# Optimization experiments

Measured on AMD Instinct MI355X. Metric: run time of the kernel, lower is better.

## Reference

```python
import jax, jax.numpy as jnp
import numpy as np

NA, NW, H = 20000, 100000, 128
DA, DW = 64, 128
E_CR, E_IN, E_CO = 400000, 600000, 300000


def _seg_softmax(logits, seg, n):
    m = jax.ops.segment_max(logits, seg, num_segments=n)
    e = jnp.exp(logits - m[seg])
    s = jax.ops.segment_sum(e, seg, num_segments=n)
    return e / (s[seg] + 1e-16)


def _gat(x_src, x_dst, edge, W, b, a_s, a_d):
    # PyG GATConv, heads=1, concat=False, shared lin for src/dst, add_self_loops=True
    n_src, n_dst = x_src.shape[0], x_dst.shape[0]
    loops = jnp.arange(min(n_src, n_dst), dtype=edge.dtype)
    src = jnp.concatenate([edge[0], loops])
    dst = jnp.concatenate([edge[1], loops])
    hs = x_src @ W            # [n_src, H]
    hd = x_dst @ W            # [n_dst, H]
    logit = jax.nn.leaky_relu((hs @ a_s)[src] + (hd @ a_d)[dst], 0.2)
    alpha = _seg_softmax(logit, dst, n_dst)          # softmax over in-neighborhoods
    out = jax.ops.segment_sum(alpha[:, None] * hs[src], dst, num_segments=n_dst)
    return out + b


def _mlp2(x, w1, b1, w2, b2):
    return jax.nn.relu(x @ w1 + b1) @ w2 + b2


def setup_inputs() -> dict:
    key = jax.random.key(0)
    ks = iter(jax.random.split(key, 40))

    def p(shape, scale=0.1):
        return jax.random.normal(next(ks), shape, jnp.float32) * scale

    def edges(n_src, n_dst, E):
        s = jax.random.randint(next(ks), (E,), 0, n_src, dtype=jnp.int32)
        d = jax.random.randint(next(ks), (E,), 0, n_dst, dtype=jnp.int32)
        d = jnp.where(s == d, (d + 1) % n_dst, d)  # keep input loop-free (PyG strips them)
        return jnp.stack([s, d])

    e_creates = edges(NA, NW, E_CR)
    inp = {
        'artist_feat': jax.random.normal(next(ks), (NA, DA), jnp.float32),
        'work_feat': jax.random.normal(next(ks), (NW, DW), jnp.float32),
        'a_w1': p((DA, H)), 'a_b1': jnp.zeros(H, jnp.float32),
        'a_w2': p((H, H)), 'a_b2': jnp.zeros(H, jnp.float32),
        'w_w1': p((DW, H)), 'w_b1': jnp.zeros(H, jnp.float32),
        'w_w2': p((H, H)), 'w_b2': jnp.zeros(H, jnp.float32),
        'cr_W': p((H, H)), 'cr_b': jnp.zeros(H, jnp.float32), 'cr_as': p((H,)), 'cr_ad': p((H,)),
        'in_W': p((H, H)), 'in_b': jnp.zeros(H, jnp.float32), 'in_as': p((H,)), 'in_ad': p((H,)),
        'co_W': p((H, H)), 'co_b': jnp.zeros(H, jnp.float32), 'co_as': p((H,)), 'co_ad': p((H,)),
        'p_w1': p((2 * H, 256)), 'p_b1': jnp.zeros(256, jnp.float32),
        'p_w2': p((256, 128)), 'p_b2': jnp.zeros(128, jnp.float32),
        'p_w3': p((128, 1)), 'p_b3': jnp.zeros(1, jnp.float32),
        'e_creates': e_creates,
        'e_created_by': jnp.flip(e_creates, axis=0),  # reverse relation [work, artist]
        'e_infl': edges(NW, NW, E_IN),
        'e_collab': edges(NA, NA, E_CO),
    }
    return inp


def reference(artist_feat, work_feat,
              a_w1, a_b1, a_w2, a_b2,
              w_w1, w_b1, w_w2, w_b2,
              cr_W, cr_b, cr_as, cr_ad,
              in_W, in_b, in_as, in_ad,
              co_W, co_b, co_as, co_ad,
              p_w1, p_b1, p_w2, p_b2, p_w3, p_b3,
              e_creates, e_created_by, e_infl, e_collab):
    ax = _mlp2(artist_feat, a_w1, a_b1, a_w2, a_b2)      # [NA, H]
    wx = _mlp2(work_feat, w_w1, w_b1, w_w2, w_b2)        # [NW, H]
    wx = jax.nn.elu(_gat(ax, wx, e_creates, cr_W, cr_b, cr_as, cr_ad))
    wx = jax.nn.elu(_gat(wx, wx, e_infl, in_W, in_b, in_as, in_ad))
    au = _gat(wx, ax, e_created_by, cr_W, cr_b, cr_as, cr_ad)  # no elu (matches source)
    ac = jax.nn.elu(_gat(au, au, e_collab, co_W, co_b, co_as, co_ad))
    comb = jnp.concatenate([au, ac], axis=1)             # [NA, 2H]
    h = jax.nn.relu(comb @ p_w1 + p_b1)                  # dropout is identity in eval
    h = jax.nn.relu(h @ p_w2 + p_b2)
    return (h @ p_w3 + p_b3).squeeze()
```

## Files before the change

### kernel.cpp

```cpp
#include <hip/hip_runtime.h>
#include <hip/hip_bf16.h>
#include <cstddef>

#define NA 20000
#define NW 100000
#define HH 128
#define DA 64
#define E_CR 400000
#define E_IN 600000
#define E_CO 300000

#define ROW1 0
#define ROW2 (NW)
#define ROW3 (2 * NW)
#define ROW4 (2 * NW + NA)
#define NTOT (2 * NW + 2 * NA)
#define CAPW 40
#define CAPA 88
#define GNB ((NA + 127) / 128)
#define NPREPG (7 * 128)

typedef short v8s __attribute__((ext_vector_type(8)));
typedef float v4f __attribute__((ext_vector_type(4)));

constexpr int PSLOT = 2 * 128 * 264;

__device__ inline short f2bf(float x) {
    union { float f; unsigned u; } c; c.f = x;
    unsigned r = c.u + 0x7fff + ((c.u >> 16) & 1);
    return (short)(r >> 16);
}
__device__ inline float bf2f(short s) {
    union { unsigned u; float f; } c; c.u = ((unsigned)(unsigned short)s) << 16;
    return c.f;
}
__device__ inline float bfu2f(unsigned short s) {
    union { unsigned u; float f; } c; c.u = ((unsigned)s) << 16;
    return c.f;
}

__device__ inline void split8(const float* xv, v8s& h, v8s& l) {
#pragma unroll
    for (int p = 0; p < 4; ++p) {
        float2 xf; xf.x = xv[2 * p]; xf.y = xv[2 * p + 1];
        __hip_bfloat162 hb = __float22bfloat162_rn(xf);
        float2 hf = __bfloat1622float2(hb);
        float2 lf; lf.x = xf.x - hf.x; lf.y = xf.y - hf.y;
        __hip_bfloat162 lb = __float22bfloat162_rn(lf);
        union { __hip_bfloat162 b; short2 s; } uh, ul;
        uh.b = hb; ul.b = lb;
        h[2 * p] = uh.s.x; h[2 * p + 1] = uh.s.y;
        l[2 * p] = ul.s.x; l[2 * p + 1] = ul.s.y;
    }
}

struct AppChunk { const int* e; int E; int* pad; int cap; int* deg; };

__device__ inline void do_append(const AppChunk& ap, int bid) {
    int b0 = bid * 1024 + threadIdx.x;
    int s[4], d[4]; bool ok[4];
#pragma unroll
    for (int u = 0; u < 4; ++u) {
        int i = b0 + u * 256;
        ok[u] = i < ap.E;
        s[u] = 0; d[u] = 0;
        if (ok[u]) { s[u] = ap.e[i]; d[u] = ap.e[ap.E + i]; }
    }
    int p[4];
#pragma unroll
    for (int u = 0; u < 4; ++u) if (ok[u]) p[u] = atomicAdd(&ap.deg[d[u]], 1);
#pragma unroll
    for (int u = 0; u < 4; ++u)
        if (ok[u] && p[u] < ap.cap)
            ap.pad[(size_t)d[u] * ap.cap + p[u]] = s[u];
}

struct PrepDesc { const float* src; int ldw; int K; };
struct PrepArgs {
    PrepDesc d[10];
    const float *wvW, *wvA;
    const float *ww2, *aw2, *wb2, *ab2;
    float *uW, *u3, *cons, *bf;
    short* wf;
    const float* gX; const float* gB; float* gY; int gM;
};

__global__ __launch_bounds__(256) void k_prep_append(PrepArgs a, short* __restrict__ out,
                                                     AppChunk ap)
{
    __shared__ short Bs2[2 * 128 * 72];
    int bx = blockIdx.x;

    if (bx == 0) {
        __shared__ float sv[HH];
        int t = threadIdx.x;
        if (t < HH) {
            float s = 0.f;
            for (int j = 0; j < HH; ++j) s += a.wvW[(size_t)t * HH + j] * a.wvA[j];
            sv[t] = s;
        }
        __syncthreads();
        if (t < HH) {
            float s = 0.f;
            for (int j = 0; j < HH; ++j) s += a.ww2[(size_t)t * HH + j] * sv[j];
            a.uW[t] = s;
        } else {
            int k = t - HH;
            float s = 0.f;
            for (int j = 0; j < HH; ++j) s += a.aw2[(size_t)k * HH + j] * sv[j];
            a.u3[k] = s;
        }
        if (t == 0) {
            float s = 0.f;
            for (int j = 0; j < HH; ++j) s += a.wb2[j] * sv[j];
            a.cons[0] = s;
        }
        if (t == 1) {
            float s = 0.f;
            for (int j = 0; j < HH; ++j) s += a.ab2[j] * sv[j];
            a.cons[1] = s;
        }
        return;
    }
    bx -= 1;
    if (bx < 4) {
        int k = bx * 32 + (threadIdx.x >> 3);
        int cb = (threadIdx.x & 7) * 16;
        for (int c = cb; c < cb + 16; ++c) {
            float s = 0.f;
            for (int j = 0; j < HH; ++j) s += a.aw2[(size_t)k * HH + j] * a.wvW[(size_t)j * HH + c];
            short h = f2bf(s);
            short l = f2bf(s - bf2f(h));
            a.wf[c * 136 + k] = h;
            a.wf[128 * 136 + c * 136 + k] = l;
        }
        if (bx == 0 && threadIdx.x < HH) {
            int c = threadIdx.x;
            float s = 0.f;
            for (int j = 0; j < HH; ++j) s += a.ab2[j] * a.wvW[(size_t)j * HH + c];
            a.bf[c] = s;
        }
        return;
    }
    bx -= 4;
    {
        int n1 = (ap.E + 1023) >> 10;
        if (bx < n1) { do_append(ap, bx); return; }
        bx -= n1;
    }
    if (bx < GNB) {
        const int bid = bx;
        const int tid = threadIdx.x;
        const int wave = tid >> 6, lane = tid & 63;
        const int l15 = lane & 15, quad = lane >> 4;
        const int wrow = bid * 128 + wave * 32;
        for (int e = tid; e < 64 * 128; e += 256) {
            int n = e & 127, k = e >> 7;
            float x = a.d[0].src[(size_t)k * 128 + n];
            short h = f2bf(x);
            short l = f2bf(x - bf2f(h));
            Bs2[n * 72 + k] = h;
            Bs2[128 * 72 + n * 72 + k] = l;
        }
        v8s ah[2][2], al[2][2];
#pragma unroll
        for (int rf = 0; rf < 2; ++rf) {
            int r = wrow + rf * 16 + l15; if (r >= a.gM) r = a.gM - 1;
            const float* xp = a.gX + (size_t)r * DA + quad * 8;
#pragma unroll
            for (int kf = 0; kf < 2; ++kf) {
                float xv[8];
                *(float4*)&xv[0] = *(const float4*)(xp + kf * 32);
                *(float4*)&xv[4] = *(const float4*)(xp + kf * 32 + 4);
                split8(xv, ah[rf][kf], al[rf][kf]);
            }
        }
        __syncthreads();
        v4f acc[2][8];
#pragma unroll
        for (int rf = 0; rf < 2; ++rf)
#pragma unroll
            for (int cf = 0; cf < 8; ++cf) acc[rf][cf] = (v4f){0.f, 0.f, 0.f, 0.f};
#pragma unroll
        for (int kf = 0; kf < 2; ++kf) {
#pragma unroll
            for (int cf = 0; cf < 8; ++cf) {
                int coff = (cf * 16 + l15) * 72 + kf * 32 + quad * 8;
                v8s bh = *(const v8s*)&Bs2[coff];
                v8s bl = *(const v8s*)&Bs2[128 * 72 + coff];
#pragma unroll
                for (int rf = 0; rf < 2; ++rf) {
                    acc[rf][cf] = __builtin_amdgcn_mfma_f32_16x16x32_bf16(al[rf][kf], bh, acc[rf][cf], 0, 0, 0);
                    acc[rf][cf] = __builtin_amdgcn_mfma_f32_16x16x32_bf16(ah[rf][kf], bl, acc[rf][cf], 0, 0, 0);
                    acc[rf][cf] = __builtin_amdgcn_mfma_f32_16x16x32_bf16(ah[rf][kf], bh, acc[rf][cf], 0, 0, 0);
                }
            }
        }
        float bv[8];
#pragma unroll
        for (int cf = 0; cf < 8; ++cf) bv[cf] = a.gB[cf * 16 + l15];
#pragma unroll
        for (int rf = 0; rf < 2; ++rf) {
#pragma unroll
            for (int reg = 0; reg < 4; ++reg) {
                int r = wrow + rf * 16 + quad * 4 + reg;
                if (r >= a.gM) continue;
                float* yp = a.gY + (size_t)r * HH;
#pragma unroll
                for (int cf = 0; cf < 8; ++cf) {
                    float o = acc[rf][cf][reg] + bv[cf];
                    yp[cf * 16 + l15] = o > 0.f ? o : 0.f;
                }
            }
        }
        return;
    }
    bx -= GNB;
    constexpr int smap[7] = {2, 4, 5, 6, 7, 8, 9};
    int m = smap[bx >> 7];
    int e = (bx & 127) * 256 + threadIdx.x;
    PrepDesc dd = a.d[m];
    int K = dd.K;
    int KP = (K <= 128) ? K + 8 : K;
    if (e >= K * 128) return;
    int n = e & 127, k = e >> 7;
    float x = dd.src[(size_t)k * dd.ldw + n];
    short h = f2bf(x);
    short l = f2bf(x - bf2f(h));
    short* base = out + (size_t)m * PSLOT;
    base[n * KP + k] = h;
    base[128 * KP + n * KP + k] = l;
}

template<int K, int ACT, int NSS, int ST, int LDSB, int OBF, int DUAL, int XBF>
__global__ __launch_bounds__(256, 4) void k_mfma(
    const float* __restrict__ X, int ldx,
    const short* __restrict__ Wp,
    const float* __restrict__ bias,
    float* __restrict__ Y, int ldy, int M,
    const float* __restrict__ v1, float* __restrict__ ss1,
    const float* __restrict__ v2, float* __restrict__ ss2,
    const float* __restrict__ sb)
{
    constexpr int KF = K / 32;
    constexpr int KP = (K <= 128) ? K + 8 : K;
    __shared__ short Bs[LDSB ? 2 * 128 * KP : 8];
    const int tid = threadIdx.x;
    const int wave = tid >> 6, lane = tid & 63;
    const int l15 = lane & 15, quad = lane >> 4;
    int bid = blockIdx.x;
    if (DUAL) {
        int g0 = gridDim.x >> 1;
        if (bid >= g0) { bid -= g0; Wp += PSLOT; bias += 128; Y += 128; }
    }
    const int wrow = bid * 128 + wave * 32;

    if (LDSB) {
        const float4* src = (const float4*)Wp;
        float4* dst = (float4*)Bs;
        constexpr int total = 2 * 128 * KP / 8;
        for (int i = tid; i < total; i += 256) dst[i] = src[i];
        __syncthreads();
    }

    v4f acc[2][8];
#pragma unroll
    for (int rf = 0; rf < 2; ++rf)
#pragma unroll
        for (int cf = 0; cf < 8; ++cf) acc[rf][cf] = (v4f){0.f, 0.f, 0.f, 0.f};

    const unsigned short* xb16[2];
    const float* xb32[2];
#pragma unroll
    for (int rf = 0; rf < 2; ++rf) {
        int r = wrow + rf * 16 + l15; if (r >= M) r = M - 1;
        xb16[rf] = (const unsigned short*)X + (size_t)r * ldx + quad * 8;
        xb32[rf] = X + (size_t)r * ldx + quad * 8;
    }

#pragma unroll
    for (int kf = 0; kf < KF; ++kf) {
        v8s ah[2], al[2];
#pragma unroll
        for (int rf = 0; rf < 2; ++rf) {
            if (XBF) {
                ah[rf] = *(const v8s*)(xb16[rf] + kf * 32);
            } else {
                float xv[8];
                *(float4*)&xv[0] = *(const float4*)(xb32[rf] + kf * 32);
                *(float4*)&xv[4] = *(const float4*)(xb32[rf] + kf * 32 + 4);
                split8(xv, ah[rf], al[rf]);
            }
        }
#pragma unroll
        for (int cf = 0; cf < 8; ++cf) {
            const short* bp = LDSB ? &Bs[(cf * 16 + l15) * KP + kf * 32 + quad * 8]
                                   : Wp + (size_t)(cf * 16 + l15) * KP + kf * 32 + quad * 8;
            v8s bh = *(const v8s*)bp;
            v8s bl = *(const v8s*)(bp + 128 * KP);
#pragma unroll
            for (int rf = 0; rf < 2; ++rf) {
                if (!XBF) acc[rf][cf] = __builtin_amdgcn_mfma_f32_16x16x32_bf16(al[rf], bh, acc[rf][cf], 0, 0, 0);
                acc[rf][cf] = __builtin_amdgcn_mfma_f32_16x16x32_bf16(ah[rf], bl, acc[rf][cf], 0, 0, 0);
                acc[rf][cf] = __builtin_amdgcn_mfma_f32_16x16x32_bf16(ah[rf], bh, acc[rf][cf], 0, 0, 0);
            }
        }
    }

    float bv[8], v1c[8], v2c[8];
#pragma unroll
    for (int cf = 0; cf < 8; ++cf) {
        int col = cf * 16 + l15;
        bv[cf] = bias ? bias[col] : 0.f;
        if (NSS >= 1) v1c[cf] = v1[col];
        if (NSS >= 2) v2c[cf] = v2[col];
    }
    float sbv = (NSS >= 1 && sb) ? sb[0] : 0.f;

#pragma unroll
    for (int rf = 0; rf < 2; ++rf) {
#pragma unroll
        for (int reg = 0; reg < 4; ++reg) {
            int r = wrow + rf * 16 + quad * 4 + reg;
            if (r >= M) continue;
            float p1 = 0.f, p2 = 0.f;
#pragma unroll
            for (int cf = 0; cf < 8; ++cf) {
                float o = acc[rf][cf][reg] + bv[cf];
                if (ACT == 1) o = o > 0.f ? o : 0.f;
                if (NSS >= 1) p1 = fmaf(o, v1c[cf], p1);
                if (NSS >= 2) p2 = fmaf(o, v2c[cf], p2);
                if (ST) {
                    if (OBF) ((unsigned short*)Y)[(size_t)r * ldy + cf * 16 + l15] = (unsigned short)f2bf(o);
                    else     Y[(size_t)r * ldy + cf * 16 + l15] = o;
                }
            }
            if (NSS >= 1) {
#pragma unroll
                for (int w = 1; w < 16; w <<= 1) {
                    p1 += __shfl_xor(p1, w, 64);
                    if (NSS >= 2) p2 += __shfl_xor(p2, w, 64);
                }
                if (l15 == 0) {
                    ss1[r] = p1 + sbv;
                    if (NSS >= 2) ss2[r] = p2;
                }
            }
        }
    }
}

struct MfmaCfg {
    const float* X; int ldx;
    const short* Wp;
    const float* bias;
    float* Y; int ldy; int M;
    int act, nss, obf, xbf, st;
    const float* v1; float* ss1;
    const float* v2; float* ss2;
    const float* sb1;
    const float* vx; float* ssx; const float* cx;
    int nblocks;
};

__global__ __launch_bounds__(256, 4) void k_mfma2(MfmaCfg c0, MfmaCfg c1, AppChunk ap)
{
    constexpr int KF = 4, KP = 136;
    const int napp = (ap.E + 1023) >> 10;
    int bid = blockIdx.x;
    if (bid < napp) { do_append(ap, bid); return; }
    bid -= napp;
    const bool first = bid < c0.nblocks;
    const MfmaCfg& c = first ? c0 : c1;
    if (!first) bid -= c0.nblocks;
    const int tid = threadIdx.x;
    const int wave = tid >> 6, lane = tid & 63;
    const int l15 = lane & 15, quad = lane >> 4;
    const int wrow = bid * 128 + wave * 32;

    v4f acc[2][8];
#pragma unroll
    for (int rf = 0; rf < 2; ++rf)
#pragma unroll
        for (int cf = 0; cf < 8; ++cf) acc[rf][cf] = (v4f){0.f, 0.f, 0.f, 0.f};

    const unsigned short* xb16[2];
    const float* xb32[2];
#pragma unroll
    for (int rf = 0; rf < 2; ++rf) {
        int r = wrow + rf * 16 + l15; if (r >= c.M) r = c.M - 1;
        xb16[rf] = (const unsigned short*)c.X + (size_t)r * c.ldx + quad * 8;
        xb32[rf] = c.X + (size_t)r * c.ldx + quad * 8;
    }

    float px[2] = {0.f, 0.f};
#pragma unroll
    for (int kf = 0; kf < KF; ++kf) {
        v8s ah[2], al[2];
        float uv[8];
        if (c.vx) {
            *(float4*)&uv[0] = *(const float4*)(c.vx + kf * 32 + quad * 8);
            *(float4*)&uv[4] = *(const float4*)(c.vx + kf * 32 + quad * 8 + 4);
        }
#pragma unroll
        for (int rf = 0; rf < 2; ++rf) {
            if (c.xbf) {
                ah[rf] = *(const v8s*)(xb16[rf] + kf * 32);
                al[rf] = (v8s)(short)0;
            } else {
                float xv[8];
                *(float4*)&xv[0] = *(const float4*)(xb32[rf] + kf * 32);
                *(float4*)&xv[4] = *(const float4*)(xb32[rf] + kf * 32 + 4);
                split8(xv, ah[rf], al[rf]);
                if (c.vx) {
#pragma unroll
                    for (int j = 0; j < 8; ++j) px[rf] = fmaf(xv[j], uv[j], px[rf]);
                }
            }
        }
#pragma unroll
        for (int cf = 0; cf < 8; ++cf) {
            const short* bp = c.Wp + (size_t)(cf * 16 + l15) * KP + kf * 32 + quad * 8;
            v8s bh = *(const v8s*)bp;
            v8s bl = *(const v8s*)(bp + 128 * KP);
#pragma unroll
            for (int rf = 0; rf < 2; ++rf) {
                if (!c.xbf) acc[rf][cf] = __builtin_amdgcn_mfma_f32_16x16x32_bf16(al[rf], bh, acc[rf][cf], 0, 0, 0);
                acc[rf][cf] = __builtin_amdgcn_mfma_f32_16x16x32_bf16(ah[rf], bl, acc[rf][cf], 0, 0, 0);
                acc[rf][cf] = __builtin_amdgcn_mfma_f32_16x16x32_bf16(ah[rf], bh, acc[rf][cf], 0, 0, 0);
            }
        }
    }

    if (c.vx) {
        float cxv = c.cx ? c.cx[0] : 0.f;
#pragma unroll
        for (int rf = 0; rf < 2; ++rf) {
            float p = px[rf];
            p += __shfl_xor(p, 16, 64);
            p += __shfl_xor(p, 32, 64);
            int rr = wrow + rf * 16 + l15;
            if (quad == 0 && rr < c.M) c.ssx[rr] = p + cxv;
        }
    }

    float bv[8], v1c[8], v2c[8];
#pragma unroll
    for (int cf = 0; cf < 8; ++cf) {
        int col = cf * 16 + l15;
        bv[cf] = c.bias ? c.bias[col] : 0.f;
        v1c[cf] = (c.nss >= 1) ? c.v1[col] : 0.f;
        v2c[cf] = (c.nss >= 2) ? c.v2[col] : 0.f;
    }
    float sbv = (c.nss >= 1 && c.sb1) ? c.sb1[0] : 0.f;

#pragma unroll
    for (int rf = 0; rf < 2; ++rf) {
#pragma unroll
        for (int reg = 0; reg < 4; ++reg) {
            int r = wrow + rf * 16 + quad * 4 + reg;
            if (r >= c.M) continue;
            float p1 = 0.f, p2 = 0.f;
#pragma unroll
            for (int cf = 0; cf < 8; ++cf) {
                float o = acc[rf][cf][reg] + bv[cf];
                if (c.act) o = o > 0.f ? o : 0.f;
                p1 = fmaf(o, v1c[cf], p1);
                p2 = fmaf(o, v2c[cf], p2);
                if (c.st) {
                    if (c.obf) ((unsigned short*)c.Y)[(size_t)r * c.ldy + cf * 16 + l15] = (unsigned short)f2bf(o);
                    else       c.Y[(size_t)r * c.ldy + cf * 16 + l15] = o;
                }
            }
            if (c.nss >= 1) {
#pragma unroll
                for (int w = 1; w < 16; w <<= 1) {
                    p1 += __shfl_xor(p1, w, 64);
                    p2 += __shfl_xor(p2, w, 64);
                }
                if (l15 == 0) {
                    c.ss1[r] = p1 + sbv;
                    if (c.nss >= 2) c.ss2[r] = p2;
                }
            }
        }
    }
}

template<int ELU, int U, int CAP, int OBF>
__global__ __launch_bounds__(256) void k_aggregate(
    const int* __restrict__ deg, const int* __restrict__ esp,
    const unsigned short* __restrict__ hs, const float* __restrict__ ss,
    const float* __restrict__ sd, const float* __restrict__ bias,
    void* __restrict__ out, int ldy, int n, int loopn)
{
    int lane = threadIdx.x & 63;
    int wv = threadIdx.x >> 6;
    int d = blockIdx.x * 4 + wv;
    if (d >= n) return;
    int half = lane >> 5;
    int col = (lane & 31) * 4;
    const int* row = esp + (size_t)d * CAP;
    int i1 = deg[d]; if (i1 > CAP) i1 = CAP;
    float sdv = sd[d];
    float den = 0.f;
    float ax = 0.f, ay = 0.f, az = 0.f, aw = 0.f;
    if (half == 0 && d < loopn) {
        ushort4 h = *(const ushort4*)(hs + (size_t)d * HH + col);
        float l = ss[d] + sdv;
        l = l < 0.f ? 0.2f * l : l;
        float e = __expf(l);
        den += e;
        ax = fmaf(e, bfu2f(h.x), ax);
        ay = fmaf(e, bfu2f(h.y), ay);
        az = fmaf(e, bfu2f(h.z), az);
        aw = fmaf(e, bfu2f(h.w), aw);
    }
    int i = 0;
    for (; i + 2 * U <= i1; i += 2 * U) {
        int s[U]; ushort4 h[U]; float sv[U];
#pragma unroll
        for (int u = 0; u < U; ++u) s[u] = row[i + 2 * u + half];
#pragma unroll
        for (int u = 0; u < U; ++u) h[u] = *(const ushort4*)(hs + (size_t)s[u] * HH + col);
#pragma unroll
        for (int u = 0; u < U; ++u) sv[u] = ss[s[u]];
#pragma unroll
        for (int u = 0; u < U; ++u) {
            float l = sv[u] + sdv;
            l = l < 0.f ? 0.2f * l : l;
            float e = __expf(l);
            den += e;
            ax = fmaf(e, bfu2f(h[u].x), ax);
            ay = fmaf(e, bfu2f(h[u].y), ay);
            az = fmaf(e, bfu2f(h[u].z), az);
            aw = fmaf(e, bfu2f(h[u].w), aw);
        }
    }
    if (i < i1) {
        int s[U]; ushort4 h[U]; float sv[U]; bool act[U];
#pragma unroll
        for (int u = 0; u < U; ++u) {
            int idx = i + 2 * u + half;
            act[u] = idx < i1;
            s[u] = row[act[u] ? idx : (i1 - 1)];
        }
#pragma unroll
        for (int u = 0; u < U; ++u) h[u] = *(const ushort4*)(hs + (size_t)s[u] * HH + col);
#pragma unroll
        for (int u = 0; u < U; ++u) sv[u] = ss[s[u]];
#pragma unroll
        for (int u = 0; u < U; ++u) {
            float l = sv[u] + sdv;
            l = l < 0.f ? 0.2f * l : l;
            float e = act[u] ? __expf(l) : 0.f;
            den += e;
            ax = fmaf(e, bfu2f(h[u].x), ax);
            ay = fmaf(e, bfu2f(h[u].y), ay);
            az = fmaf(e, bfu2f(h[u].z), az);
            aw = fmaf(e, bfu2f(h[u].w), aw);
        }
    }
    den += __shfl_xor(den, 32, 64);
    ax += __shfl_xor(ax, 32, 64);
    ay += __shfl_xor(ay, 32, 64);
    az += __shfl_xor(az, 32, 64);
    aw += __shfl_xor(aw, 32, 64);
    if (half == 0) {
        float4 b = *(const float4*)(bias + col);
        float inv = 1.f / (den + 1e-16f);
        float o0 = ax * inv + b.x;
        float o1 = ay * inv + b.y;
        float o2 = az * inv + b.z;
        float o3 = aw * inv + b.w;
        if (ELU) {
            o0 = o0 > 0.f ? o0 : expm1f(o0);
            o1 = o1 > 0.f ? o1 : expm1f(o1);
            o2 = o2 > 0.f ? o2 : expm1f(o2);
            o3 = o3 > 0.f ? o3 : expm1f(o3);
        }
        if (OBF) {
            ushort4 ob;
            ob.x = (unsigned short)f2bf(o0);
            ob.y = (unsigned short)f2bf(o1);
            ob.z = (unsigned short)f2bf(o2);
            ob.w = (unsigned short)f2bf(o3);
            *(ushort4*)((unsigned short*)out + (size_t)d * ldy + col) = ob;
        } else {
            *(float4*)((float*)out + (size_t)d * ldy + col) = make_float4(o0, o1, o2, o3);
        }
    }
}

extern "C" void kernel_launch(void* const* d_in, const int* in_sizes, int n_in,
                              void* d_out, int out_size, void* d_ws, size_t ws_size,
                              hipStream_t stream)
{
    const float* artist = (const float*)d_in[0];
    const float* workf  = (const float*)d_in[1];
    const float* a_w1 = (const float*)d_in[2];  const float* a_b1 = (const float*)d_in[3];
    const float* a_w2 = (const float*)d_in[4];  const float* a_b2 = (const float*)d_in[5];
    const float* w_w1 = (const float*)d_in[6];  const float* w_b1 = (const float*)d_in[7];
    const float* w_w2 = (const float*)d_in[8];  const float* w_b2 = (const float*)d_in[9];
    const float* cr_W = (const float*)d_in[10]; const float* cr_b = (const float*)d_in[11];
    const float* cr_as = (const float*)d_in[12]; const float* cr_ad = (const float*)d_in[13];
    const float* in_W = (const float*)d_in[14]; const float* in_b = (const float*)d_in[15];
    const float* in_as = (const float*)d_in[16]; const float* in_ad = (const float*)d_in[17];
    const float* co_W = (const float*)d_in[18]; const float* co_b = (const float*)d_in[19];
    const float* co_as = (const float*)d_in[20]; const float* co_ad = (const float*)d_in[21];
    const float* p_w1 = (const float*)d_in[22]; const float* p_b1 = (const float*)d_in[23];
    const float* p_w2 = (const float*)d_in[24]; const float* p_b2 = (const float*)d_in[25];
    const float* p_w3 = (const float*)d_in[26]; const float* p_b3 = (const float*)d_in[27];
    const int* e_cr = (const int*)d_in[28];
    const int* e_cb = (const int*)d_in[29];
    const int* e_in = (const int*)d_in[30];
    const int* e_co = (const int*)d_in[31];

    char* wsp = (char*)d_ws;
    size_t off = 0;
    auto alloc = [&](size_t bytes) -> void* {
        void* p = wsp + off;
        off += (bytes + 255) / 256 * 256;
        return p;
    };
    float* hsA  = (float*)alloc((size_t)NA * HH * 4);
    unsigned short* wxb = (unsigned short*)alloc((size_t)NW * HH * 2);
    unsigned short* hsb = (unsigned short*)alloc((size_t)NW * HH * 2);
    float* h1   = (float*)alloc((size_t)NA * 256 * 4);
    float* comb = (float*)alloc((size_t)NA * 256 * 4);
    float* ss1 = (float*)alloc((size_t)NA * 4);
    float* sd1 = (float*)alloc((size_t)NW * 4);
    float* ss2 = (float*)alloc((size_t)NW * 4);
    float* sd2 = (float*)alloc((size_t)NW * 4);
    float* ss3 = (float*)alloc((size_t)NW * 4);
    float* sd3 = (float*)alloc((size_t)NA * 4);
    float* ss4 = (float*)alloc((size_t)NA * 4);
    float* sd4 = (float*)alloc((size_t)NA * 4);
    float* uW  = (float*)alloc(HH * 4);
    float* u3v = (float*)alloc(HH * 4);
    float* bfv = (float*)alloc(HH * 4);
    float* cons = (float*)alloc(2 * 4);
    int* deg   = (int*)alloc((size_t)NTOT * 4);
    int* pad1  = (int*)alloc((size_t)NW * CAPW * 4);
    int* pad2  = (int*)alloc((size_t)NW * CAPW * 4);
    int* pad3  = (int*)alloc((size_t)NA * CAPA * 4);
    int* pad4  = (int*)alloc((size_t)NA * CAPA * 4);
    short* preW = (short*)alloc((size_t)10 * PSLOT * 2);
    (void)ws_size; (void)in_sizes; (void)n_in; (void)out_size;

    auto pre = [&](int m) { return preW + (size_t)m * PSLOT; };
    auto gg = [](int M) { return (M + 127) / 128; };
    auto apb = [](int E) { return (E + 1023) / 1024; };
    const float* nf = nullptr;
    float* nfm = nullptr;

    PrepArgs pa;
    pa.d[0] = {a_w1, HH, DA};
    pa.d[1] = {a_w2, HH, HH};
    pa.d[2] = {w_w1, HH, HH};
    pa.d[3] = {w_w2, HH, HH};
    pa.d[4] = {cr_W, HH, HH};
    pa.d[5] = {in_W, HH, HH};
    pa.d[6] = {co_W, HH, HH};
    pa.d[7] = {p_w1, 256, 256};
    pa.d[8] = {p_w1 + 128, 256, 256};
    pa.d[9] = {p_w2, HH, 256};
    pa.wvW = cr_W; pa.wvA = cr_ad;
    pa.ww2 = w_w2; pa.aw2 = a_w2; pa.wb2 = w_b2; pa.ab2 = a_b2;
    pa.uW = uW; pa.u3 = u3v; pa.cons = cons; pa.bf = bfv;
    pa.wf = pre(1);
    pa.gX = artist; pa.gB = a_b1; pa.gY = hsA; pa.gM = NA;

    AppChunk ap1 = {e_cr, E_CR, pad1, CAPW, deg + ROW1};
    AppChunk ap2 = {e_in, E_IN, pad2, CAPW, deg + ROW2};
    AppChunk ap3 = {e_cb, E_CR, pad3, CAPA, deg + ROW3};
    AppChunk ap4 = {e_co, E_CO, pad4, CAPA, deg + ROW4};
    AppChunk ap0 = {nullptr, 0, nullptr, 1, nullptr};

    (void)hipMemsetAsync(deg, 0, (size_t)NTOT * 4, stream);

    {
        int nblk = 5 + apb(E_CR) + GNB + NPREPG;
        k_prep_append<<<nblk, 256, 0, stream>>>(pa, preW, ap1);
    }

    {
        MfmaCfg c0 = {workf, HH, pre(2), w_b1, nullptr, HH, NW,
                      1, 1, 0, 0, 0,
                      uW, sd1, nf, nfm,
                      cons,
                      nf, nfm, nf,
                      gg(NW)};
        MfmaCfg c1 = {hsA, HH, pre(1), bfv, (float*)hsb, HH, NA,
                      0, 1, 1, 0, 1,
                      cr_as, ss1, nf, nfm,
                      nf,
                      u3v, sd3, cons + 1,
                      gg(NA)};
        k_mfma2<<<apb(E_IN) + gg(NW) + gg(NA), 256, 0, stream>>>(c0, c1, ap2);
    }

    k_aggregate<1, 2, CAPW, 1><<<(NW + 3) / 4, 256, 0, stream>>>(deg + ROW1, pad1, hsb, ss1, sd1, cr_b, wxb, HH, NW, NA);

    {
        MfmaCfg c0 = {(const float*)wxb, HH, pre(5), nullptr, (float*)hsb, HH, NW,
                      0, 2, 1, 1, 1,
                      in_as, ss2, in_ad, sd2,
                      nf, nf, nfm, nf,
                      gg(NW)};
        MfmaCfg c1 = c0; c1.nblocks = 0;
        k_mfma2<<<apb(E_CR) + gg(NW), 256, 0, stream>>>(c0, c1, ap3);
    }
    k_aggregate<1, 2, CAPW, 1><<<(NW + 3) / 4, 256, 0, stream>>>(deg + ROW2, pad2, hsb, ss2, sd2, in_b, wxb, HH, NW, NW);

    {
        MfmaCfg c0 = {(const float*)wxb, HH, pre(4), nullptr, (float*)hsb, HH, NW,
                      0, 1, 1, 1, 1,
                      cr_as, ss3, nf, nfm,
                      nf, nf, nfm, nf,
                      gg(NW)};
        MfmaCfg c1 = c0; c1.nblocks = 0;
        k_mfma2<<<apb(E_CO) + gg(NW), 256, 0, stream>>>(c0, c1, ap4);
    }
    k_aggregate<0, 4, CAPA, 0><<<(NA + 3) / 4, 256, 0, stream>>>(deg + ROW3, pad3, hsb, ss3, sd3, cr_b, comb, 256, NA, NA);

    k_mfma<HH, 0, 2, 1, 0, 1, 0, 0><<<gg(NA), 256, 0, stream>>>(comb, 256, pre(6), nullptr, (float*)hsb, HH, NA, co_as, ss4, co_ad, sd4, nf);
    k_aggregate<1, 4, CAPA, 0><<<(NA + 3) / 4, 256, 0, stream>>>(deg + ROW4, pad4, hsb, ss4, sd4, co_b, comb + 128, 256, NA, NA);

    k_mfma<256, 1, 0, 1, 0, 0, 1, 0><<<2 * gg(NA), 256, 0, stream>>>(comb, 256, pre(7), p_b1, h1, 256, NA, nf, nfm, nf, nfm, nf);
    k_mfma<256, 1, 1, 0, 0, 0, 0, 0><<<gg(NA), 256, 0, stream>>>(h1, 256, pre(9), p_b2, nfm, 0, NA, p_w3, (float*)d_out, nf, nfm, p_b3);
    (void)ap0;
}
```

Baseline: 683.0 us.

## Stage weights in LDS, preload activations, and reorder block roles in fused kernels

```diff
diff --git a/kernel.cpp b/kernel.cpp
--- a/kernel.cpp
+++ b/kernel.cpp
@@ -17,8 +17,8 @@
 #define NTOT (2 * NW + 2 * NA)
 #define CAPW 40
 #define CAPA 88
+#define NPREP (10 * 128 + 1)
 #define GNB ((NA + 127) / 128)
-#define NPREPG (7 * 128)
 
 typedef short v8s __attribute__((ext_vector_type(8)));
 typedef float v4f __attribute__((ext_vector_type(4)));
@@ -86,45 +86,13 @@
 };
 
 __global__ __launch_bounds__(256) void k_prep_append(PrepArgs a, short* __restrict__ out,
-                                                     AppChunk ap)
+                                                    AppChunk ap)
 {
     __shared__ short Bs2[2 * 128 * 72];
-    int bx = blockIdx.x;
-
-    if (bx == 0) {
-        __shared__ float sv[HH];
-        int t = threadIdx.x;
-        if (t < HH) {
-            float s = 0.f;
-            for (int j = 0; j < HH; ++j) s += a.wvW[(size_t)t * HH + j] * a.wvA[j];
-            sv[t] = s;
-        }
-        __syncthreads();
-        if (t < HH) {
-            float s = 0.f;
-            for (int j = 0; j < HH; ++j) s += a.ww2[(size_t)t * HH + j] * sv[j];
-            a.uW[t] = s;
-        } else {
-            int k = t - HH;
-            float s = 0.f;
-            for (int j = 0; j < HH; ++j) s += a.aw2[(size_t)k * HH + j] * sv[j];
-            a.u3[k] = s;
-        }
-        if (t == 0) {
-            float s = 0.f;
-            for (int j = 0; j < HH; ++j) s += a.wb2[j] * sv[j];
-            a.cons[0] = s;
-        }
-        if (t == 1) {
-            float s = 0.f;
-            for (int j = 0; j < HH; ++j) s += a.ab2[j] * sv[j];
-            a.cons[1] = s;
-        }
-        return;
-    }
-    bx -= 1;
-    if (bx < 4) {
-        int k = bx * 32 + (threadIdx.x >> 3);
+    const int napp = (ap.E + 1023) >> 10;
+    if ((int)blockIdx.x >= NPREP + GNB + napp) {
+        int idx = blockIdx.x - (NPREP + GNB + napp);
+        int k = idx * 32 + (threadIdx.x >> 3);
         int cb = (threadIdx.x & 7) * 16;
         for (int c = cb; c < cb + 16; ++c) {
             float s = 0.f;
@@ -134,7 +102,7 @@
             a.wf[c * 136 + k] = h;
             a.wf[128 * 136 + c * 136 + k] = l;
         }
-        if (bx == 0 && threadIdx.x < HH) {
+        if (idx == 0 && threadIdx.x < HH) {
             int c = threadIdx.x;
             float s = 0.f;
             for (int j = 0; j < HH; ++j) s += a.ab2[j] * a.wvW[(size_t)j * HH + c];
@@ -142,14 +110,9 @@
         }
         return;
     }
-    bx -= 4;
-    {
-        int n1 = (ap.E + 1023) >> 10;
-        if (bx < n1) { do_append(ap, bx); return; }
-        bx -= n1;
-    }
-    if (bx < GNB) {
-        const int bid = bx;
+    if (blockIdx.x >= NPREP + GNB) { do_append(ap, blockIdx.x - NPREP - GNB); return; }
+    if (blockIdx.x >= NPREP) {
+        int bid = blockIdx.x - NPREP;
         const int tid = threadIdx.x;
         const int wave = tid >> 6, lane = tid & 63;
         const int l15 = lane & 15, quad = lane >> 4;
@@ -215,10 +178,39 @@
         }
         return;
     }
-    bx -= GNB;
-    constexpr int smap[7] = {2, 4, 5, 6, 7, 8, 9};
-    int m = smap[bx >> 7];
-    int e = (bx & 127) * 256 + threadIdx.x;
+    if (blockIdx.x == NPREP - 1) {
+        __shared__ float sv[HH];
+        int t = threadIdx.x;
+        if (t < HH) {
+            float s = 0.f;
+            for (int j = 0; j < HH; ++j) s += a.wvW[(size_t)t * HH + j] * a.wvA[j];
+            sv[t] = s;
+        }
+        __syncthreads();
+        if (t < HH) {
+            float s = 0.f;
+            for (int j = 0; j < HH; ++j) s += a.ww2[(size_t)t * HH + j] * sv[j];
+            a.uW[t] = s;
+        } else {
+            int k = t - HH;
+            float s = 0.f;
+            for (int j = 0; j < HH; ++j) s += a.aw2[(size_t)k * HH + j] * sv[j];
+            a.u3[k] = s;
+        }
+        if (t == 0) {
+            float s = 0.f;
+            for (int j = 0; j < HH; ++j) s += a.wb2[j] * sv[j];
+            a.cons[0] = s;
+        }
+        if (t == 1) {
+            float s = 0.f;
+            for (int j = 0; j < HH; ++j) s += a.ab2[j] * sv[j];
+            a.cons[1] = s;
+        }
+        return;
+    }
+    int m = blockIdx.x >> 7;
+    int e = (blockIdx.x & 127) * 256 + threadIdx.x;
     PrepDesc dd = a.d[m];
     int K = dd.K;
     int KP = (K <= 128) ? K + 8 : K;
@@ -233,7 +225,7 @@
 }
 
 template<int K, int ACT, int NSS, int ST, int LDSB, int OBF, int DUAL, int XBF>
-__global__ __launch_bounds__(256, 4) void k_mfma(
+__global__ __launch_bounds__(256, 2) void k_mfma(
     const float* __restrict__ X, int ldx,
     const short* __restrict__ Wp,
     const float* __restrict__ bias,
@@ -243,8 +235,8 @@
     const float* __restrict__ sb)
 {
     constexpr int KF = K / 32;
-    constexpr int KP = (K <= 128) ? K + 8 : K;
-    __shared__ short Bs[LDSB ? 2 * 128 * KP : 8];
+    constexpr int KP = LDSB ? K + 8 : K;
+    __shared__ short Bs[LDSB ? 2 * 128 * (K + 8) : 8];
     const int tid = threadIdx.x;
     const int wave = tid >> 6, lane = tid & 63;
     const int l15 = lane & 15, quad = lane >> 4;
@@ -260,7 +252,6 @@
         float4* dst = (float4*)Bs;
         constexpr int total = 2 * 128 * KP / 8;
         for (int i = tid; i < total; i += 256) dst[i] = src[i];
-        __syncthreads();
     }
 
     v4f acc[2][8];
@@ -269,40 +260,40 @@
 #pragma unroll
         for (int cf = 0; cf < 8; ++cf) acc[rf][cf] = (v4f){0.f, 0.f, 0.f, 0.f};
 
-    const unsigned short* xb16[2];
-    const float* xb32[2];
+    v8s ah[2][KF], al[2][KF];
 #pragma unroll
     for (int rf = 0; rf < 2; ++rf) {
         int r = wrow + rf * 16 + l15; if (r >= M) r = M - 1;
-        xb16[rf] = (const unsigned short*)X + (size_t)r * ldx + quad * 8;
-        xb32[rf] = X + (size_t)r * ldx + quad * 8;
-    }
-
+        if (XBF) {
+            const unsigned short* xp = (const unsigned short*)X + (size_t)r * ldx + quad * 8;
+#pragma unroll
+            for (int kf = 0; kf < KF; ++kf)
+                ah[rf][kf] = *(const v8s*)(xp + kf * 32);
+        } else {
+            const float* xp = X + (size_t)r * ldx + quad * 8;
+#pragma unroll
+            for (int kf = 0; kf < KF; ++kf) {
+                float xv[8];
+                *(float4*)&xv[0] = *(const float4*)(xp + kf * 32);
+                *(float4*)&xv[4] = *(const float4*)(xp + kf * 32 + 4);
+                split8(xv, ah[rf][kf], al[rf][kf]);
+            }
+        }
+    }
+    if (LDSB) __syncthreads();
 #pragma unroll
     for (int kf = 0; kf < KF; ++kf) {
-        v8s ah[2], al[2];
-#pragma unroll
-        for (int rf = 0; rf < 2; ++rf) {
-            if (XBF) {
-                ah[rf] = *(const v8s*)(xb16[rf] + kf * 32);
-            } else {
-                float xv[8];
-                *(float4*)&xv[0] = *(const float4*)(xb32[rf] + kf * 32);
-                *(float4*)&xv[4] = *(const float4*)(xb32[rf] + kf * 32 + 4);
-                split8(xv, ah[rf], al[rf]);
-            }
-        }
 #pragma unroll
         for (int cf = 0; cf < 8; ++cf) {
             const short* bp = LDSB ? &Bs[(cf * 16 + l15) * KP + kf * 32 + quad * 8]
-                                   : Wp + (size_t)(cf * 16 + l15) * KP + kf * 32 + quad * 8;
+                                   : Wp + (size_t)(cf * 16 + l15) * K + kf * 32 + quad * 8;
             v8s bh = *(const v8s*)bp;
             v8s bl = *(const v8s*)(bp + 128 * KP);
 #pragma unroll
             for (int rf = 0; rf < 2; ++rf) {
-                if (!XBF) acc[rf][cf] = __builtin_amdgcn_mfma_f32_16x16x32_bf16(al[rf], bh, acc[rf][cf], 0, 0, 0);
-                acc[rf][cf] = __builtin_amdgcn_mfma_f32_16x16x32_bf16(ah[rf], bl, acc[rf][cf], 0, 0, 0);
-                acc[rf][cf] = __builtin_amdgcn_mfma_f32_16x16x32_bf16(ah[rf], bh, acc[rf][cf], 0, 0, 0);
+                if (!XBF) acc[rf][cf] = __builtin_amdgcn_mfma_f32_16x16x32_bf16(al[rf][kf], bh, acc[rf][cf], 0, 0, 0);
+                acc[rf][cf] = __builtin_amdgcn_mfma_f32_16x16x32_bf16(ah[rf][kf], bl, acc[rf][cf], 0, 0, 0);
+                acc[rf][cf] = __builtin_amdgcn_mfma_f32_16x16x32_bf16(ah[rf][kf], bh, acc[rf][cf], 0, 0, 0);
             }
         }
     }
@@ -363,13 +354,13 @@
     int nblocks;
 };
 
-__global__ __launch_bounds__(256, 4) void k_mfma2(MfmaCfg c0, MfmaCfg c1, AppChunk ap)
+__global__ __launch_bounds__(256, 2) void k_mfma2(MfmaCfg c0, MfmaCfg c1, AppChunk ap)
 {
     constexpr int KF = 4, KP = 136;
-    const int napp = (ap.E + 1023) >> 10;
+    __shared__ short Bs[2 * 128 * KP];
     int bid = blockIdx.x;
-    if (bid < napp) { do_append(ap, bid); return; }
-    bid -= napp;
+    const int ngemm = c0.nblocks + c1.nblocks;
+    if (bid >= ngemm) { do_append(ap, bid - ngemm); return; }
     const bool first = bid < c0.nblocks;
     const MfmaCfg& c = first ? c0 : c1;
     if (!first) bid -= c0.nblocks;
@@ -378,56 +369,62 @@
     const int l15 = lane & 15, quad = lane >> 4;
     const int wrow = bid * 128 + wave * 32;
 
+    {
+        const float4* src = (const float4*)c.Wp;
+        float4* dst = (float4*)Bs;
+        constexpr int total = 2 * 128 * KP / 8;
+        for (int i = tid; i < total; i += 256) dst[i] = src[i];
+    }
+
     v4f acc[2][8];
 #pragma unroll
     for (int rf = 0; rf < 2; ++rf)
 #pragma unroll
         for (int cf = 0; cf < 8; ++cf) acc[rf][cf] = (v4f){0.f, 0.f, 0.f, 0.f};
 
-    const unsigned short* xb16[2];
-    const float* xb32[2];
+    v8s ah[2][KF], al[2][KF];
+    float px[2] = {0.f, 0.f};
 #pragma unroll
     for (int rf = 0; rf < 2; ++rf) {
         int r = wrow + rf * 16 + l15; if (r >= c.M) r = c.M - 1;
-        xb16[rf] = (const unsigned short*)c.X + (size_t)r * c.ldx + quad * 8;
-        xb32[rf] = c.X + (size_t)r * c.ldx + quad * 8;
-    }
-
-    float px[2] = {0.f, 0.f};
+        if (c.xbf) {
+            const unsigned short* xp = (const unsigned short*)c.X + (size_t)r * c.ldx + quad * 8;
+#pragma unroll
+            for (int kf = 0; kf < KF; ++kf) {
+                ah[rf][kf] = *(const v8s*)(xp + kf * 32);
+                al[rf][kf] = (v8s)(short)0;
+            }
+        } else {
+            const float* xp = c.X + (size_t)r * c.ldx + quad * 8;
+#pragma unroll
+            for (int kf = 0; kf < KF; ++kf) {
+                float xv[8];
+                *(float4*)&xv[0] = *(const float4*)(xp + kf * 32);
+                *(float4*)&xv[4] = *(const float4*)(xp + kf * 32 + 4);
+                split8(xv, ah[rf][kf], al[rf][kf]);
+                if (c.vx) {
+                    float uv[8];
+                    *(float4*)&uv[0] = *(const float4*)(c.vx + kf * 32 + quad * 8);
+                    *(float4*)&uv[4] = *(const float4*)(c.vx + kf * 32 + quad * 8 + 4);
+#pragma unroll
+                    for (int j = 0; j < 8; ++j) px[rf] = fmaf(xv[j], uv[j], px[rf]);
+                }
+            }
+        }
+    }
+    __syncthreads();
 #pragma unroll
     for (int kf = 0; kf < KF; ++kf) {
-        v8s ah[2], al[2];
-        float uv[8];
-        if (c.vx) {
-            *(float4*)&uv[0] = *(const float4*)(c.vx + kf * 32 + quad * 8);
-            *(float4*)&uv[4] = *(const float4*)(c.vx + kf * 32 + quad * 8 + 4);
-        }
-#pragma unroll
-        for (int rf = 0; rf < 2; ++rf) {
-            if (c.xbf) {
-                ah[rf] = *(const v8s*)(xb16[rf] + kf * 32);
-                al[rf] = (v8s)(short)0;
-            } else {
-                float xv[8];
-                *(float4*)&xv[0] = *(const float4*)(xb32[rf] + kf * 32);
-                *(float4*)&xv[4] = *(const float4*)(xb32[rf] + kf * 32 + 4);
-                split8(xv, ah[rf], al[rf]);
-                if (c.vx) {
-#pragma unroll
-                    for (int j = 0; j < 8; ++j) px[rf] = fmaf(xv[j], uv[j], px[rf]);
-                }
-            }
-        }
 #pragma unroll
         for (int cf = 0; cf < 8; ++cf) {
-            const short* bp = c.Wp + (size_t)(cf * 16 + l15) * KP + kf * 32 + quad * 8;
+            const short* bp = &Bs[(cf * 16 + l15) * KP + kf * 32 + quad * 8];
             v8s bh = *(const v8s*)bp;
             v8s bl = *(const v8s*)(bp + 128 * KP);
 #pragma unroll
             for (int rf = 0; rf < 2; ++rf) {
-                if (!c.xbf) acc[rf][cf] = __builtin_amdgcn_mfma_f32_16x16x32_bf16(al[rf], bh, acc[rf][cf], 0, 0, 0);
-                acc[rf][cf] = __builtin_amdgcn_mfma_f32_16x16x32_bf16(ah[rf], bl, acc[rf][cf], 0, 0, 0);
-                acc[rf][cf] = __builtin_amdgcn_mfma_f32_16x16x32_bf16(ah[rf], bh, acc[rf][cf], 0, 0, 0);
+                if (!c.xbf) acc[rf][cf] = __builtin_amdgcn_mfma_f32_16x16x32_bf16(al[rf][kf], bh, acc[rf][cf], 0, 0, 0);
+                acc[rf][cf] = __builtin_amdgcn_mfma_f32_16x16x32_bf16(ah[rf][kf], bl, acc[rf][cf], 0, 0, 0);
+                acc[rf][cf] = __builtin_amdgcn_mfma_f32_16x16x32_bf16(ah[rf][kf], bh, acc[rf][cf], 0, 0, 0);
             }
         }
     }
@@ -645,7 +642,7 @@
     int* pad2  = (int*)alloc((size_t)NW * CAPW * 4);
     int* pad3  = (int*)alloc((size_t)NA * CAPA * 4);
     int* pad4  = (int*)alloc((size_t)NA * CAPA * 4);
-    short* preW = (short*)alloc((size_t)10 * PSLOT * 2);
+    short* preW = (short*)alloc((size_t)11 * PSLOT * 2);
     (void)ws_size; (void)in_sizes; (void)n_in; (void)out_size;
 
     auto pre = [&](int m) { return preW + (size_t)m * PSLOT; };
@@ -668,21 +665,17 @@
     pa.wvW = cr_W; pa.wvA = cr_ad;
     pa.ww2 = w_w2; pa.aw2 = a_w2; pa.wb2 = w_b2; pa.ab2 = a_b2;
     pa.uW = uW; pa.u3 = u3v; pa.cons = cons; pa.bf = bfv;
-    pa.wf = pre(1);
+    pa.wf = pre(10);
     pa.gX = artist; pa.gB = a_b1; pa.gY = hsA; pa.gM = NA;
 
     AppChunk ap1 = {e_cr, E_CR, pad1, CAPW, deg + ROW1};
     AppChunk ap2 = {e_in, E_IN, pad2, CAPW, deg + ROW2};
     AppChunk ap3 = {e_cb, E_CR, pad3, CAPA, deg + ROW3};
     AppChunk ap4 = {e_co, E_CO, pad4, CAPA, deg + ROW4};
-    AppChunk ap0 = {nullptr, 0, nullptr, 1, nullptr};
 
     (void)hipMemsetAsync(deg, 0, (size_t)NTOT * 4, stream);
 
-    {
-        int nblk = 5 + apb(E_CR) + GNB + NPREPG;
-        k_prep_append<<<nblk, 256, 0, stream>>>(pa, preW, ap1);
-    }
+    k_prep_append<<<NPREP + GNB + apb(E_CR) + 4, 256, 0, stream>>>(pa, preW, ap1);
 
     {
         MfmaCfg c0 = {workf, HH, pre(2), w_b1, nullptr, HH, NW,
@@ -691,13 +684,13 @@
                       cons,
                       nf, nfm, nf,
                       gg(NW)};
-        MfmaCfg c1 = {hsA, HH, pre(1), bfv, (float*)hsb, HH, NA,
+        MfmaCfg c1 = {hsA, HH, pre(10), bfv, (float*)hsb, HH, NA,
                       0, 1, 1, 0, 1,
                       cr_as, ss1, nf, nfm,
                       nf,
                       u3v, sd3, cons + 1,
                       gg(NA)};
-        k_mfma2<<<apb(E_IN) + gg(NW) + gg(NA), 256, 0, stream>>>(c0, c1, ap2);
+        k_mfma2<<<gg(NW) + gg(NA) + apb(E_IN), 256, 0, stream>>>(c0, c1, ap2);
     }
 
     k_aggregate<1, 2, CAPW, 1><<<(NW + 3) / 4, 256, 0, stream>>>(deg + ROW1, pad1, hsb, ss1, sd1, cr_b, wxb, HH, NW, NA);
@@ -709,7 +702,7 @@
                       nf, nf, nfm, nf,
                       gg(NW)};
         MfmaCfg c1 = c0; c1.nblocks = 0;
-        k_mfma2<<<apb(E_CR) + gg(NW), 256, 0, stream>>>(c0, c1, ap3);
+        k_mfma2<<<gg(NW) + apb(E_CO), 256, 0, stream>>>(c0, c1, ap4);
     }
     k_aggregate<1, 2, CAPW, 1><<<(NW + 3) / 4, 256, 0, stream>>>(deg + ROW2, pad2, hsb, ss2, sd2, in_b, wxb, HH, NW, NW);
 
@@ -720,14 +713,13 @@
                       nf, nf, nfm, nf,
                       gg(NW)};
         MfmaCfg c1 = c0; c1.nblocks = 0;
-        k_mfma2<<<apb(E_CO) + gg(NW), 256, 0, stream>>>(c0, c1, ap4);
+        k_mfma2<<<gg(NW) + apb(E_CR), 256, 0, stream>>>(c0, c1, ap3);
     }
     k_aggregate<0, 4, CAPA, 0><<<(NA + 3) / 4, 256, 0, stream>>>(deg + ROW3, pad3, hsb, ss3, sd3, cr_b, comb, 256, NA, NA);
 
-    k_mfma<HH, 0, 2, 1, 0, 1, 0, 0><<<gg(NA), 256, 0, stream>>>(comb, 256, pre(6), nullptr, (float*)hsb, HH, NA, co_as, ss4, co_ad, sd4, nf);
+    k_mfma<HH, 0, 2, 1, 1, 1, 0, 0><<<gg(NA), 256, 0, stream>>>(comb, 256, pre(6), nullptr, (float*)hsb, HH, NA, co_as, ss4, co_ad, sd4, nf);
     k_aggregate<1, 4, CAPA, 0><<<(NA + 3) / 4, 256, 0, stream>>>(deg + ROW4, pad4, hsb, ss4, sd4, co_b, comb + 128, 256, NA, NA);
 
     k_mfma<256, 1, 0, 1, 0, 0, 1, 0><<<2 * gg(NA), 256, 0, stream>>>(comb, 256, pre(7), p_b1, h1, 256, NA, nf, nfm, nf, nfm, nf);
     k_mfma<256, 1, 1, 0, 0, 0, 0, 0><<<gg(NA), 256, 0, stream>>>(h1, 256, pre(9), p_b2, nfm, 0, NA, p_w3, (float*)d_out, nf, nfm, p_b3);
-    (void)ap0;
-}
+}
```

After: 681.0 us. Within noise of the previous version (-0.3%).
